# Kernel tuning notes

Measured on AMD Instinct MI355X. Metric: run time of the kernel, lower is better.

## Reference

```python
import jax, jax.numpy as jnp
import numpy as np

V_TH = 1.0       # v_threshold
INIT_TAU = 2.0   # raw tau; decay = sigmoid(INIT_TAU)
T, B, IN_SZ, OUT_SZ = 32, 128, 2048, 2048


def setup_inputs() -> dict:
    key = jax.random.key(0)
    k1, k2 = jax.random.split(key)
    x = jax.random.normal(k1, (T, B, IN_SZ), jnp.float32)
    kernel = jax.random.normal(k2, (IN_SZ, OUT_SZ), jnp.float32) / np.sqrt(IN_SZ)
    return {"x": x, "kernel": kernel}


def reference(x, kernel):
    """Forward of Approx_OTPE's inner SNN step (f), scanned over time and
    vmapped over batch. Cell: u' = sigmoid(init_tau)*u + x @ W;
    s = heaviside(u' - v_th); soft reset u_out = u' - s*v_th.
    Returns stacked spikes [T, B, OUT_SZ]."""
    sig_tau = jax.nn.sigmoid(jnp.asarray(INIT_TAU, x.dtype))
    _, batch, _ = x.shape
    out_sz = kernel.shape[1]
    u0 = jnp.zeros((batch, out_sz), x.dtype)

    def body(u, xt):
        u_next = sig_tau * u + xt @ kernel          # [B, O]
        s = (u_next >= V_TH).astype(x.dtype)        # spike_fn forward
        u_out = u_next - s * V_TH                   # soft reset
        return u_out, s

    _, spikes = jax.lax.scan(body, u0, x)
    return spikes
```

## Files before the change

kernel.cpp:

```cpp
#include <hip/hip_runtime.h>
#include <math.h>

constexpr int T_STEPS = 32;
constexpr int BATCH   = 128;
constexpr int IN_SZ   = 2048;
constexpr int OUT_SZ  = 2048;

__global__ __launch_bounds__(256, 1) void Approx_OTPE_67181878444197_kernel(
        const float* __restrict__ x,
        const float* __restrict__ W,
        float* __restrict__ out) {
    constexpr int BK = 16, BM = 128, BN = 64, BB = 4;
    constexpr int YSTR = BN + 1;

    __shared__ float smem[BM * YSTR];
    float* const As = smem;
    float* const Bs = smem + BK * BM;

    const int o0  = blockIdx.x * BN;
    const int b0  = blockIdx.y * BB;
    const int tid = threadIdx.x;
    const int ty  = tid >> 4;
    const int tx  = tid & 15;

    const int am  = tid >> 1;
    const int akq = (tid & 1) * 8;
    const int at  = am >> 2;
    const int ab  = am & 3;
    const size_t aBase = ((size_t)at * BATCH + (size_t)(b0 + ab)) * IN_SZ + akq;

    const int brow = tid >> 4;
    const int bcol = (tid & 15) * 4;

    float acc[8][4] = {};
    float su[8][4]  = {};

    for (int k0 = 0; k0 < IN_SZ; k0 += BK) {
        const float4 av0 = *reinterpret_cast<const float4*>(&x[aBase + k0]);
        const float4 av1 = *reinterpret_cast<const float4*>(&x[aBase + k0 + 4]);
        const float4 bv  = *reinterpret_cast<const float4*>(
            &W[(size_t)(k0 + brow) * OUT_SZ + o0 + bcol]);

        if (k0 == 512 || k0 == 1024 || k0 == 1536) {
            #pragma unroll
            for (int i = 0; i < 8; ++i)
                #pragma unroll
                for (int j = 0; j < 4; ++j) {
                    su[i][j]  = __fadd_rn(su[i][j], acc[i][j]);
                    acc[i][j] = 0.0f;
                }
        }

        __syncthreads();
        As[(akq + 0) * BM + am] = av0.x;
        As[(akq + 1) * BM + am] = av0.y;
        As[(akq + 2) * BM + am] = av0.z;
        As[(akq + 3) * BM + am] = av0.w;
        As[(akq + 4) * BM + am] = av1.x;
        As[(akq + 5) * BM + am] = av1.y;
        As[(akq + 6) * BM + am] = av1.z;
        As[(akq + 7) * BM + am] = av1.w;
        *reinterpret_cast<float4*>(&Bs[brow * BN + bcol]) = bv;
        __syncthreads();

        #pragma unroll
        for (int k = 0; k < BK; ++k) {
            const float4 a0 = *reinterpret_cast<const float4*>(&As[k * BM + ty * 8]);
            const float4 a1 = *reinterpret_cast<const float4*>(&As[k * BM + ty * 8 + 4]);
            const float4 wf = *reinterpret_cast<const float4*>(&Bs[k * BN + tx * 4]);
            const float a[8] = {a0.x, a0.y, a0.z, a0.w, a1.x, a1.y, a1.z, a1.w};
            const float w[4] = {wf.x, wf.y, wf.z, wf.w};
            #pragma unroll
            for (int i = 0; i < 8; ++i)
                #pragma unroll
                for (int j = 0; j < 4; ++j)
                    acc[i][j] = __builtin_fmaf(a[i], w[j], acc[i][j]);
        }
    }

    __syncthreads();
    #pragma unroll
    for (int i = 0; i < 8; ++i)
        #pragma unroll
        for (int j = 0; j < 4; ++j)
            smem[(ty * 8 + i) * YSTR + tx * 4 + j] = __fadd_rn(su[i][j], acc[i][j]);
    __syncthreads();

    {
        const int bl = tid >> 6;
        const int o  = tid & 63;
        const size_t plane  = (size_t)BATCH * OUT_SZ;
        const size_t outIdx = (size_t)(b0 + bl) * OUT_SZ + o0 + o;

        const double D = 1.0 / (1.0 + exp(-2.0));
        double u = 0.0;
        #pragma unroll
        for (int t = 0; t < T_STEPS; ++t) {
            const double y  = (double)smem[(t * 4 + bl) * YSTR + o];
            const double un = __dadd_rn(__dmul_rn(D, u), y);
            const double s  = (un >= 1.0) ? 1.0 : 0.0;
            u = __dsub_rn(un, s);
            out[(size_t)t * plane + outIdx] = (float)s;
        }
    }
}

extern "C" void kernel_launch(void* const* d_in, const int* in_sizes, int n_in,
                              void* d_out, int out_size, void* d_ws, size_t ws_size,
                              hipStream_t stream) {
    const float* x = (const float*)d_in[0];
    const float* W = (const float*)d_in[1];
    float* out     = (float*)d_out;

    dim3 grid(OUT_SZ / 64, BATCH / 4);
    Approx_OTPE_67181878444197_kernel<<<grid, 256, 0, stream>>>(x, W, out);
}
```

Before: 479.4 us.

## Halve batch tile per block to double grid and use 128-thread blocks

Each block now covers 2 batch rows instead of 4, with 128 threads and a 64-row A tile, so the grid doubles to 2048 blocks. Each thread loads two float4 of W per stage. The epilogue stages the accumulators through a smaller shared buffer in two halves of 16 timesteps each, keeping the membrane recurrence in registers. The aim is more parallel blocks and less shared memory per block, traded for half the reuse of each W tile, which doubles W traffic.

```diff
diff --git a/kernel.cpp b/kernel.cpp
--- a/kernel.cpp
+++ b/kernel.cpp
@@ -6,42 +6,47 @@
 constexpr int IN_SZ   = 2048;
 constexpr int OUT_SZ  = 2048;
 
-__global__ __launch_bounds__(256, 1) void Approx_OTPE_67181878444197_kernel(
+__global__ __launch_bounds__(128, 1) void Approx_OTPE_67181878444197_kernel(
         const float* __restrict__ x,
         const float* __restrict__ W,
         float* __restrict__ out) {
-    constexpr int BK = 16, BM = 128, BN = 64, BB = 4;
+    constexpr int BK = 16, BM = 64, BN = 64;
     constexpr int YSTR = BN + 1;
+    constexpr int YSZ  = 32 * YSTR;
 
-    __shared__ float smem[BM * YSTR];
+    __shared__ float smem[YSZ];
     float* const As = smem;
     float* const Bs = smem + BK * BM;
 
     const int o0  = blockIdx.x * BN;
-    const int b0  = blockIdx.y * BB;
+    const int b0  = blockIdx.y * 2;
     const int tid = threadIdx.x;
     const int ty  = tid >> 4;
     const int tx  = tid & 15;
 
-    const int am  = tid >> 1;
-    const int akq = (tid & 1) * 8;
-    const int at  = am >> 2;
-    const int ab  = am & 3;
-    const size_t aBase = ((size_t)at * BATCH + (size_t)(b0 + ab)) * IN_SZ + akq;
+    const int am = tid >> 1;
+    const int ak = (tid & 1) * 8;
+    const int at = am >> 1;
+    const int ab = am & 1;
+    const size_t aBase = ((size_t)at * BATCH + (size_t)(b0 + ab)) * IN_SZ + ak;
 
-    const int brow = tid >> 4;
-    const int bcol = (tid & 15) * 4;
+    const int br = tid >> 3;
+    const int bc = (tid & 7) * 8;
 
     float acc[8][4] = {};
     float su[8][4]  = {};
 
-    for (int k0 = 0; k0 < IN_SZ; k0 += BK) {
-        const float4 av0 = *reinterpret_cast<const float4*>(&x[aBase + k0]);
-        const float4 av1 = *reinterpret_cast<const float4*>(&x[aBase + k0 + 4]);
-        const float4 bv  = *reinterpret_cast<const float4*>(
-            &W[(size_t)(k0 + brow) * OUT_SZ + o0 + bcol]);
+    #pragma unroll 1
+    for (int it = 0; it < IN_SZ / BK; ++it) {
+        const int k0 = it * BK;
+        const float4 a0 = *reinterpret_cast<const float4*>(&x[aBase + k0]);
+        const float4 a1 = *reinterpret_cast<const float4*>(&x[aBase + k0 + 4]);
+        const float4 v0 = *reinterpret_cast<const float4*>(
+            &W[(size_t)(k0 + br) * OUT_SZ + o0 + bc]);
+        const float4 v1 = *reinterpret_cast<const float4*>(
+            &W[(size_t)(k0 + br) * OUT_SZ + o0 + bc + 4]);
 
-        if (k0 == 512 || k0 == 1024 || k0 == 1536) {
+        if (it == 32 || it == 64 || it == 96) {
             #pragma unroll
             for (int i = 0; i < 8; ++i)
                 #pragma unroll
@@ -52,23 +57,24 @@
         }
 
         __syncthreads();
-        As[(akq + 0) * BM + am] = av0.x;
-        As[(akq + 1) * BM + am] = av0.y;
-        As[(akq + 2) * BM + am] = av0.z;
-        As[(akq + 3) * BM + am] = av0.w;
-        As[(akq + 4) * BM + am] = av1.x;
-        As[(akq + 5) * BM + am] = av1.y;
-        As[(akq + 6) * BM + am] = av1.z;
-        As[(akq + 7) * BM + am] = av1.w;
-        *reinterpret_cast<float4*>(&Bs[brow * BN + bcol]) = bv;
+        As[(ak + 0) * BM + am] = a0.x;
+        As[(ak + 1) * BM + am] = a0.y;
+        As[(ak + 2) * BM + am] = a0.z;
+        As[(ak + 3) * BM + am] = a0.w;
+        As[(ak + 4) * BM + am] = a1.x;
+        As[(ak + 5) * BM + am] = a1.y;
+        As[(ak + 6) * BM + am] = a1.z;
+        As[(ak + 7) * BM + am] = a1.w;
+        *reinterpret_cast<float4*>(&Bs[br * BN + bc])     = v0;
+        *reinterpret_cast<float4*>(&Bs[br * BN + bc + 4]) = v1;
         __syncthreads();
 
         #pragma unroll
         for (int k = 0; k < BK; ++k) {
-            const float4 a0 = *reinterpret_cast<const float4*>(&As[k * BM + ty * 8]);
-            const float4 a1 = *reinterpret_cast<const float4*>(&As[k * BM + ty * 8 + 4]);
+            const float4 x0 = *reinterpret_cast<const float4*>(&As[k * BM + ty * 8]);
+            const float4 x1 = *reinterpret_cast<const float4*>(&As[k * BM + ty * 8 + 4]);
             const float4 wf = *reinterpret_cast<const float4*>(&Bs[k * BN + tx * 4]);
-            const float a[8] = {a0.x, a0.y, a0.z, a0.w, a1.x, a1.y, a1.z, a1.w};
+            const float a[8] = {x0.x, x0.y, x0.z, x0.w, x1.x, x1.y, x1.z, x1.w};
             const float w[4] = {wf.x, wf.y, wf.z, wf.w};
             #pragma unroll
             for (int i = 0; i < 8; ++i)
@@ -78,25 +84,35 @@
         }
     }
 
-    __syncthreads();
     #pragma unroll
     for (int i = 0; i < 8; ++i)
         #pragma unroll
         for (int j = 0; j < 4; ++j)
-            smem[(ty * 8 + i) * YSTR + tx * 4 + j] = __fadd_rn(su[i][j], acc[i][j]);
-    __syncthreads();
+            su[i][j] = __fadd_rn(su[i][j], acc[i][j]);
 
-    {
-        const int bl = tid >> 6;
-        const int o  = tid & 63;
-        const size_t plane  = (size_t)BATCH * OUT_SZ;
-        const size_t outIdx = (size_t)(b0 + bl) * OUT_SZ + o0 + o;
+    const int bl = tid >> 6;
+    const int o  = tid & 63;
+    const size_t plane  = (size_t)BATCH * OUT_SZ;
+    const size_t outIdx = (size_t)(b0 + bl) * OUT_SZ + o0 + o;
+    const double D = 1.0 / (1.0 + exp(-2.0));
+    double u = 0.0;
 
-        const double D = 1.0 / (1.0 + exp(-2.0));
-        double u = 0.0;
+    #pragma unroll
+    for (int p = 0; p < 2; ++p) {
+        __syncthreads();
+        if ((ty >> 2) == p) {
+            const int rb = ty * 8 - p * 32;
+            #pragma unroll
+            for (int i = 0; i < 8; ++i)
+                #pragma unroll
+                for (int j = 0; j < 4; ++j)
+                    smem[(rb + i) * YSTR + tx * 4 + j] = su[i][j];
+        }
+        __syncthreads();
         #pragma unroll
-        for (int t = 0; t < T_STEPS; ++t) {
-            const double y  = (double)smem[(t * 4 + bl) * YSTR + o];
+        for (int tt = 0; tt < 16; ++tt) {
+            const int t = p * 16 + tt;
+            const double y  = (double)smem[(tt * 2 + bl) * YSTR + o];
             const double un = __dadd_rn(__dmul_rn(D, u), y);
             const double s  = (un >= 1.0) ? 1.0 : 0.0;
             u = __dsub_rn(un, s);
@@ -112,6 +128,6 @@
     const float* W = (const float*)d_in[1];
     float* out     = (float*)d_out;
 
-    dim3 grid(OUT_SZ / 64, BATCH / 4);
-    Approx_OTPE_67181878444197_kernel<<<grid, 256, 0, stream>>>(x, W, out);
+    dim3 grid(OUT_SZ / 64, BATCH / 2);
+    Approx_OTPE_67181878444197_kernel<<<grid, 128, 0, stream>>>(x, W, out);
 }
```

Result: slower. 515.4 us (+7.5%).
